# Performance work log

Hardware: AMD Instinct MI355X
Metric: run time of the kernel (lower is better)

The kernel has to match this reference:

```python
import jax, jax.numpy as jnp
import numpy as np

EMBED_DIM = 1024
NUM_HEADS = 16
HEAD_DIM = EMBED_DIM // NUM_HEADS


def setup_inputs() -> dict:
    key = jax.random.key(0)
    ks = jax.random.split(key, 9)
    s = 1.0 / np.sqrt(EMBED_DIM)
    X = jax.random.normal(ks[0], (4, 2048, EMBED_DIM), dtype=jnp.float32)
    # Linear weights stored as [in, out] for x @ W + b
    Wq = jax.random.uniform(ks[1], (EMBED_DIM, EMBED_DIM), jnp.float32, -s, s)
    bq = jax.random.uniform(ks[2], (EMBED_DIM,), jnp.float32, -s, s)
    Wk = jax.random.uniform(ks[3], (EMBED_DIM, EMBED_DIM), jnp.float32, -s, s)
    bk = jax.random.uniform(ks[4], (EMBED_DIM,), jnp.float32, -s, s)
    Wv = jax.random.uniform(ks[5], (EMBED_DIM, EMBED_DIM), jnp.float32, -s, s)
    bv = jax.random.uniform(ks[6], (EMBED_DIM,), jnp.float32, -s, s)
    Wo = jax.random.uniform(ks[7], (EMBED_DIM, EMBED_DIM), jnp.float32, -s, s)
    bo = jax.random.uniform(ks[8], (EMBED_DIM,), jnp.float32, -s, s)
    return {"X": X, "Wq": Wq, "bq": bq, "Wk": Wk, "bk": bk,
            "Wv": Wv, "bv": bv, "Wo": Wo, "bo": bo}


def reference(X, Wq, bq, Wk, bk, Wv, bv, Wo, bo):
    B, S, _ = X.shape
    def split_heads(t):  # [B,S,E] -> [B,H,S,D]
        return t.reshape(B, S, NUM_HEADS, HEAD_DIM).transpose(0, 2, 1, 3)
    Q = split_heads(X @ Wq + bq)
    K = split_heads(X @ Wk + bk)
    V = split_heads(X @ Wv + bv)
    scale = 1.0 / np.sqrt(HEAD_DIM).astype(np.float32)
    scores = jnp.einsum('bhqd,bhkd->bhqk', Q, K) * scale
    probs = jax.nn.softmax(scores, axis=-1)
    attn = jnp.einsum('bhqk,bhkd->bhqd', probs, V)  # [B,H,S,D]
    combined = attn.transpose(0, 2, 1, 3).reshape(B, S, EMBED_DIM)
    return combined @ Wo + bo
```

## Files before the change

kernel.cpp:

```cpp
#include <hip/hip_runtime.h>
#include <hip/hip_bf16.h>

#define EMBED 1024
#define NHEADS 16
#define HDIM 64
#define SEQ 2048
#define BATCH 4
#define ROWS (BATCH * SEQ)

typedef __attribute__((ext_vector_type(8))) short bf16x8;
typedef __attribute__((ext_vector_type(4))) float f32x4;
typedef __attribute__((ext_vector_type(2))) float f32x2;
typedef __attribute__((ext_vector_type(16))) float f32x16;
typedef __attribute__((ext_vector_type(4))) unsigned int u32x4;
typedef __attribute__((ext_vector_type(2))) unsigned int u32x2;
typedef __attribute__((ext_vector_type(2))) int i32x2;
typedef unsigned int u32;

#define SL2E 0.18033688011112042f

__device__ __forceinline__ short f2bf(float f) {
    u32 u = __builtin_bit_cast(u32, f) + 0x8000u;
    return (short)(u >> 16);
}

__device__ __forceinline__ u32 pkbf(float a, float b) {
    u32 ua = __builtin_bit_cast(u32, a) + 0x8000u;
    u32 ub = __builtin_bit_cast(u32, b) + 0x8000u;
    return __builtin_amdgcn_perm(ua, ub, 0x03020706u);
}

__device__ __forceinline__ float fexp2(float x) {
#if __has_builtin(__builtin_amdgcn_exp2f)
    return __builtin_amdgcn_exp2f(x);
#else
    return exp2f(x);
#endif
}

__device__ __forceinline__ void async16(const void* g, void* l) {
    __builtin_amdgcn_global_load_lds((const __attribute__((address_space(1))) u32*)g,
                                     (__attribute__((address_space(3))) u32*)l, 16, 0, 0);
}

__global__ __launch_bounds__(256) void convert_f32_bf16(const float* __restrict__ in,
                                                        short* __restrict__ out) {
    int i = (blockIdx.x * 256 + threadIdx.x) * 4;
    float4 v = *(const float4*)&in[i];
    u32x2 o = { pkbf(v.x, v.y), pkbf(v.z, v.w) };
    *(u32x2*)&out[i] = o;
}

__global__ __launch_bounds__(256) void transpose_w4(const float* __restrict__ W0,
                                                    const float* __restrict__ W1,
                                                    const float* __restrict__ W2,
                                                    const float* __restrict__ W3,
                                                    short* __restrict__ T0,
                                                    short* __restrict__ T1,
                                                    short* __restrict__ T2,
                                                    short* __restrict__ T3) {
    const int z = blockIdx.z;
    const float* W = (z == 0) ? W0 : (z == 1) ? W1 : (z == 2) ? W2 : W3;
    short* WT = (z == 0) ? T0 : (z == 1) ? T1 : (z == 2) ? T2 : T3;
    const float sc = (z == 0) ? SL2E : 1.0f;
    __shared__ float T[64][65];
    const int k0 = blockIdx.y * 64, n0 = blockIdx.x * 64;
    const int rr = threadIdx.x >> 4, cc = (threadIdx.x & 15) * 4;
    #pragma unroll
    for (int p = 0; p < 4; ++p) {
        int r = p * 16 + rr;
        float4 v = *(const float4*)&W[(size_t)(k0 + r) * EMBED + n0 + cc];
        T[r][cc] = v.x * sc; T[r][cc + 1] = v.y * sc; T[r][cc + 2] = v.z * sc; T[r][cc + 3] = v.w * sc;
    }
    __syncthreads();
    #pragma unroll
    for (int p = 0; p < 4; ++p) {
        int r = p * 16 + rr;
        u32x2 o = { pkbf(T[cc][r], T[cc + 1][r]), pkbf(T[cc + 2][r], T[cc + 3][r]) };
        *(u32x2*)&WT[(size_t)(n0 + r) * EMBED + k0 + cc] = o;
    }
}

__global__ __launch_bounds__(512, 2) void gemm256(const short* __restrict__ A,
                                                  const short* __restrict__ BT,
                                                  const float* __restrict__ b0,
                                                  const float* __restrict__ b1,
                                                  const float* __restrict__ b2,
                                                  void* __restrict__ C0,
                                                  void* __restrict__ C1,
                                                  void* __restrict__ C2,
                                                  int mode) {
    __shared__ short As[2][16384];
    __shared__ short Bs[2][16384];
    const int tid = threadIdx.x;
    const int wid = tid >> 6, lane = tid & 63;
    const int c16 = lane & 15, quad = lane >> 4, sw = c16 & 7;
    const int wm = wid >> 2, wn = wid & 3;
    const int rowblk = blockIdx.y * 256, colblk = blockIdx.x * 256;

    const int r0 = tid >> 3;
    const int g0 = (tid & 7) ^ (r0 & 7);
    const short* aS0 = A + (size_t)(rowblk + r0) * EMBED + g0 * 8;
    const short* bS0 = BT + (size_t)(colblk + r0) * EMBED + g0 * 8;

#define STAGE_A(SBUF, H, V) do { \
    const short* _s = aS0 + (size_t)(H) * 131072 + (V) * 64; \
    async16(_s,         &As[SBUF][(H) * 8192 + wid * 512]); \
    async16(_s + 65536, &As[SBUF][(H) * 8192 + wid * 512 + 4096]); \
} while (0)
#define STAGE_B(SBUF, H, V) do { \
    const short* _s = bS0 + (size_t)(H) * 131072 + (V) * 64; \
    async16(_s,         &Bs[SBUF][(H) * 8192 + wid * 512]); \
    async16(_s + 65536, &Bs[SBUF][(H) * 8192 + wid * 512 + 4096]); \
} while (0)

    f32x4 acc[8][4] = {};

#define PHASE(BUF, MH, NH, SAB, SBUF, SH, SV, VM) do { \
    bf16x8 af[4][2], bfv[2][2]; \
    _Pragma("unroll") \
    for (int fm = 0; fm < 4; ++fm) { \
        const int row = (MH) * 128 + wm * 64 + fm * 16 + c16; \
        _Pragma("unroll") \
        for (int ks = 0; ks < 2; ++ks) \
            af[fm][ks] = *(const bf16x8*)&As[BUF][row * 64 + ((ks * 4 + quad) ^ sw) * 8]; \
    } \
    _Pragma("unroll") \
    for (int fn = 0; fn < 2; ++fn) { \
        const int rowb = (NH) * 128 + wn * 32 + fn * 16 + c16; \
        _Pragma("unroll") \
        for (int ks = 0; ks < 2; ++ks) \
            bfv[fn][ks] = *(const bf16x8*)&Bs[BUF][rowb * 64 + ((ks * 4 + quad) ^ sw) * 8]; \
    } \
    if ((SAB) == 0) STAGE_A(SBUF, SH, SV); else STAGE_B(SBUF, SH, SV); \
    __builtin_amdgcn_s_barrier(); \
    asm volatile("s_waitcnt lgkmcnt(0)" ::: "memory"); \
    __builtin_amdgcn_s_setprio(1); \
    _Pragma("unroll") \
    for (int fm = 0; fm < 4; ++fm) \
        _Pragma("unroll") \
        for (int fn = 0; fn < 2; ++fn) \
            _Pragma("unroll") \
            for (int ks = 0; ks < 2; ++ks) \
                acc[(MH) * 4 + fm][(NH) * 2 + fn] = \
                    __builtin_amdgcn_mfma_f32_16x16x32_bf16(af[fm][ks], bfv[fn][ks], \
                        acc[(MH) * 4 + fm][(NH) * 2 + fn], 0, 0, 0); \
    __builtin_amdgcn_s_setprio(0); \
    if (VM) asm volatile("s_waitcnt vmcnt(4)" ::: "memory"); \
    __builtin_amdgcn_s_barrier(); \
} while (0)

    STAGE_A(0, 0, 0); STAGE_B(0, 0, 0);
    STAGE_A(0, 1, 0); STAGE_B(0, 1, 0);
    STAGE_A(1, 0, 1); STAGE_B(1, 0, 1);
    asm volatile("s_waitcnt vmcnt(4)" ::: "memory");
    __builtin_amdgcn_s_barrier();

    #pragma unroll 1
    for (int it = 0; it < 8; ++it) {
        const int u = 2 * it;
        const int v1 = u + 1, v2 = (u + 2) & 15, v3 = (u + 3) & 15;
        PHASE(0, 0, 0, 0, 1, 1, v1, 0);
        PHASE(0, 0, 1, 1, 1, 1, v1, 0);
        PHASE(0, 1, 0, 0, 0, 0, v2, 0);
        PHASE(0, 1, 1, 1, 0, 0, v2, 1);
        PHASE(1, 0, 0, 0, 0, 1, v2, 0);
        PHASE(1, 0, 1, 1, 0, 1, v2, 0);
        PHASE(1, 1, 0, 0, 1, 0, v3, 0);
        PHASE(1, 1, 1, 1, 1, 0, v3, 1);
    }

    asm volatile("s_waitcnt vmcnt(0)" ::: "memory");

    const int rb0 = rowblk + wm * 64 + quad * 4;
    const int cb0 = wn * 32 + c16;
    if (mode == 0) {
        const int z = colblk >> 10;
        const int cm = colblk & 1023;
        const float* bias = (z == 0) ? b0 : (z == 1) ? b1 : b2;
        if (z == 2) {
            short* Vt = (short*)C2;
            #pragma unroll
            for (int m = 0; m < 8; ++m) {
                const int row = rb0 + (m >> 2) * 128 + (m & 3) * 16;
                const int b = row >> 11, s = row & 2047;
                #pragma unroll
                for (int n = 0; n < 4; ++n) {
                    const int cv = cm + cb0 + (n >> 1) * 128 + (n & 1) * 16;
                    const int head = cv >> 6, d = cv & 63;
                    const float bv = bias[cv];
                    u32x2 o = { pkbf(acc[m][n][0] + bv, acc[m][n][1] + bv),
                                pkbf(acc[m][n][2] + bv, acc[m][n][3] + bv) };
                    *(u32x2*)&Vt[((size_t)(b * NHEADS + head) * HDIM + d) * SEQ + s] = o;
                }
            }
        } else {
            short* Cq = (short*)((z == 0) ? C0 : C1);
            const float bsc = (z == 0) ? SL2E : 1.0f;
            #pragma unroll
            for (int m = 0; m < 8; ++m) {
                const int row = rb0 + (m >> 2) * 128 + (m & 3) * 16;
                #pragma unroll
                for (int n = 0; n < 4; ++n) {
                    const int col = cm + cb0 + (n >> 1) * 128 + (n & 1) * 16;
                    const float bv = bias[col] * bsc;
                    #pragma unroll
                    for (int r = 0; r < 4; ++r)
                        Cq[(size_t)(row + r) * EMBED + col] = f2bf(acc[m][n][r] + bv);
                }
            }
        }
    } else {
        float* Co = (float*)C0;
        #pragma unroll
        for (int m = 0; m < 8; ++m) {
            const int row = rb0 + (m >> 2) * 128 + (m & 3) * 16;
            #pragma unroll
            for (int n = 0; n < 4; ++n) {
                const int col = colblk + cb0 + (n >> 1) * 128 + (n & 1) * 16;
                const float bv = b0[col];
                #pragma unroll
                for (int r = 0; r < 4; ++r)
                    Co[(size_t)(row + r) * EMBED + col] = acc[m][n][r] + bv;
            }
        }
    }
#undef PHASE
#undef STAGE_A
#undef STAGE_B
}

__global__ __launch_bounds__(256, 3) void attn_mfma(const short* __restrict__ Qb,
                                                    const short* __restrict__ Kb,
                                                    const short* __restrict__ Vt,
                                                    short* __restrict__ Ob) {
    __shared__ short SH[8192];
    short* Ks = SH;
    short* Vs = SH + 4096;
    const int tid = threadIdx.x;
    const int wave = tid >> 6, lane = tid & 63;
    const int l31 = lane & 31, h = lane >> 5;
    const int swz = l31 & 7;
    const int bh = blockIdx.y;
    const int b = bh >> 4, hd = bh & 15;
    const size_t base = (size_t)b * SEQ * EMBED + (size_t)hd * HDIM;
    const size_t vbase = (size_t)bh * HDIM * SEQ;
    const int q0 = blockIdx.x * 128;

    bf16x8 qf[4];
    #pragma unroll
    for (int ks = 0; ks < 4; ++ks)
        qf[ks] = *(const bf16x8*)&Qb[base + (size_t)(q0 + wave * 32 + l31) * EMBED + ks * 16 + h * 8];

    const short* kp[2];
    const short* vp[2];
    int ldofs[2];
    #pragma unroll
    for (int it = 0; it < 2; ++it) {
        int ci = (it * 4 + wave) * 64 + lane;
        int row = ci >> 3, g = (ci & 7) ^ (row & 7);
        kp[it] = Kb + base + (size_t)row * EMBED + g * 8;
        vp[it] = Vt + vbase + (size_t)row * SEQ + g * 8;
        ldofs[it] = (it * 4 + wave) * 512;
    }

    f32x16 O[2] = {};
    f32x2 ls = {0.0f, 0.0f};

    for (int kt = 0; kt < SEQ / 64; ++kt) {
        #pragma unroll
        for (int it = 0; it < 2; ++it) {
            async16(kp[it], &Ks[ldofs[it]]);
            async16(vp[it], &Vs[ldofs[it]]);
            kp[it] += 64 * EMBED;
            vp[it] += 64;
        }
        __syncthreads();

        f32x16 st[2] = {};
        #pragma unroll
        for (int nt = 0; nt < 2; ++nt)
            #pragma unroll
            for (int ks = 0; ks < 4; ++ks) {
                bf16x8 ak = *(const bf16x8*)&Ks[(nt * 32 + l31) * 64 + ((ks * 2 + h) ^ swz) * 8];
                st[nt] = __builtin_amdgcn_mfma_f32_32x32x16_bf16(ak, qf[ks], st[nt], 0, 0, 0);
            }

        u32 pk[2][8];
        #pragma unroll
        for (int nt = 0; nt < 2; ++nt)
            #pragma unroll
            for (int i = 0; i < 8; ++i) {
                float e0 = fexp2(st[nt][2 * i]), e1 = fexp2(st[nt][2 * i + 1]);
                f32x2 e = { e0, e1 };
                ls += e;
                pk[nt][i] = pkbf(e0, e1);
            }

        #pragma unroll
        for (int ks = 0; ks < 4; ++ks) {
            const int nt = ks >> 1, bs = (ks & 1) * 4;
            u32x4 fr;
#if __has_builtin(__builtin_amdgcn_permlane32_swap)
            i32x2 sA = __builtin_amdgcn_permlane32_swap((int)pk[nt][bs + 0], (int)pk[nt][bs + 2], false, false);
            i32x2 sB = __builtin_amdgcn_permlane32_swap((int)pk[nt][bs + 1], (int)pk[nt][bs + 3], false, false);
            fr.x = (u32)sA.x; fr.y = (u32)sB.x; fr.z = (u32)sA.y; fr.w = (u32)sB.y;
#else
            u32 s0 = h ? pk[nt][bs + 0] : pk[nt][bs + 2];
            u32 s1 = h ? pk[nt][bs + 1] : pk[nt][bs + 3];
            u32 r0 = (u32)__shfl_xor((int)s0, 32);
            u32 r1 = (u32)__shfl_xor((int)s1, 32);
            fr.x = h ? r0 : pk[nt][bs + 0];
            fr.y = h ? r1 : pk[nt][bs + 1];
            fr.z = h ? pk[nt][bs + 2] : r0;
            fr.w = h ? pk[nt][bs + 3] : r1;
#endif
            bf16x8 pf = __builtin_bit_cast(bf16x8, fr);
            #pragma unroll
            for (int mt = 0; mt < 2; ++mt) {
                bf16x8 vf = *(const bf16x8*)&Vs[(mt * 32 + l31) * 64 + ((ks * 2 + h) ^ swz) * 8];
                O[mt] = __builtin_amdgcn_mfma_f32_32x32x16_bf16(vf, pf, O[mt], 0, 0, 0);
            }
        }
        __syncthreads();
    }

    float lsum = ls.x + ls.y;
    lsum += __shfl_xor(lsum, 32);
    float inv = 1.0f / lsum;

    const int wbase = wave * 2048;
    #pragma unroll
    for (int mt = 0; mt < 2; ++mt)
        #pragma unroll
        for (int m = 0; m < 4; ++m) {
            u32x2 wv;
            wv.x = pkbf(O[mt][4 * m + 0] * inv, O[mt][4 * m + 1] * inv);
            wv.y = pkbf(O[mt][4 * m + 2] * inv, O[mt][4 * m + 3] * inv);
            int u = mt * 8 + 2 * m + h;
            int su = u ^ ((l31 & 7) << 1);
            *(u32x2*)&SH[wbase + l31 * 64 + su * 4] = wv;
        }
    __syncthreads();
    #pragma unroll
    for (int p = 0; p < 4; ++p) {
        int ci = p * 256 + tid;
        int wq = ci >> 8, rem = ci & 255;
        int r = rem >> 3, cch = rem & 7;
        int su = (2 * cch) ^ ((r & 7) << 1);
        bf16x8 val = *(const bf16x8*)&SH[wq * 2048 + r * 64 + su * 4];
        *(bf16x8*)&Ob[base + (size_t)(q0 + wq * 32 + r) * EMBED + cch * 8] = val;
    }
}

extern "C" void kernel_launch(void* const* d_in, const int* in_sizes, int n_in,
                              void* d_out, int out_size, void* d_ws, size_t ws_size,
                              hipStream_t stream)
{
    const float* X  = (const float*)d_in[0];
    const float* Wq = (const float*)d_in[1];
    const float* bq = (const float*)d_in[2];
    const float* Wk = (const float*)d_in[3];
    const float* bk = (const float*)d_in[4];
    const float* Wv = (const float*)d_in[5];
    const float* bv = (const float*)d_in[6];
    const float* Wo = (const float*)d_in[7];
    const float* bo = (const float*)d_in[8];
    float* out = (float*)d_out;

    const size_t NE = (size_t)ROWS * EMBED;
    short* Xbf = (short*)d_ws;
    short* Qb  = Xbf + NE;
    short* Kb  = Qb + NE;
    short* Vtb = Kb + NE;
    short* WqT = Vtb + NE;
    short* WkT = WqT + (size_t)EMBED * EMBED;
    short* WvT = WkT + (size_t)EMBED * EMBED;
    short* WoT = WvT + (size_t)EMBED * EMBED;

    convert_f32_bf16<<<(ROWS * EMBED) / 1024, 256, 0, stream>>>(X, Xbf);
    dim3 gw(16, 16, 4);
    transpose_w4<<<gw, 256, 0, stream>>>(Wq, Wk, Wv, Wo, WqT, WkT, WvT, WoT);

    dim3 gq(12, 32, 1);
    gemm256<<<gq, 512, 0, stream>>>(Xbf, WqT, bq, bk, bv, Qb, Kb, Vtb, 0);

    dim3 gt(SEQ / 128, BATCH * NHEADS);
    attn_mfma<<<gt, 256, 0, stream>>>(Qb, Kb, Vtb, Qb);

    dim3 gg(4, 32, 1);
    gemm256<<<gg, 512, 0, stream>>>(Qb, WoT, bo, bo, bo, out, out, out, 1);
}
```

Before: 311.3 us.

## Reorder GEMM phases to reuse A/B fragments and use 128x64 kernel for output projection

Restructures the 256x256 GEMM main loop so that A and B register fragments are loaded once and reused across consecutive MFMA phases (even/odd B buffers, snake order), with adjusted staging order and vmcnt depth. This cuts LDS reads per phase. The output projection now uses a new simpler 128x64-tile kernel with more blocks (16x64 grid) instead of the 4x32 grid of 256-tiles, to improve CU occupancy for the smaller GEMM. The new kernel has no software pipelining and may be less efficient per tile.

```diff
diff --git a/kernel.cpp b/kernel.cpp
--- a/kernel.cpp
+++ b/kernel.cpp
@@ -115,59 +115,65 @@
 } while (0)
 
     f32x4 acc[8][4] = {};
-
-#define PHASE(BUF, MH, NH, SAB, SBUF, SH, SV, VM) do { \
-    bf16x8 af[4][2], bfv[2][2]; \
+    bf16x8 aU[4][2], bE[2][2], bO[2][2];
+
+#define LDA(BUF, MH) do { \
     _Pragma("unroll") \
     for (int fm = 0; fm < 4; ++fm) { \
         const int row = (MH) * 128 + wm * 64 + fm * 16 + c16; \
         _Pragma("unroll") \
         for (int ks = 0; ks < 2; ++ks) \
-            af[fm][ks] = *(const bf16x8*)&As[BUF][row * 64 + ((ks * 4 + quad) ^ sw) * 8]; \
+            aU[fm][ks] = *(const bf16x8*)&As[BUF][row * 64 + ((ks * 4 + quad) ^ sw) * 8]; \
     } \
+} while (0)
+#define LDB(BUF, NH, DST) do { \
     _Pragma("unroll") \
     for (int fn = 0; fn < 2; ++fn) { \
         const int rowb = (NH) * 128 + wn * 32 + fn * 16 + c16; \
         _Pragma("unroll") \
         for (int ks = 0; ks < 2; ++ks) \
-            bfv[fn][ks] = *(const bf16x8*)&Bs[BUF][rowb * 64 + ((ks * 4 + quad) ^ sw) * 8]; \
+            DST[fn][ks] = *(const bf16x8*)&Bs[BUF][rowb * 64 + ((ks * 4 + quad) ^ sw) * 8]; \
     } \
-    if ((SAB) == 0) STAGE_A(SBUF, SH, SV); else STAGE_B(SBUF, SH, SV); \
-    __builtin_amdgcn_s_barrier(); \
-    asm volatile("s_waitcnt lgkmcnt(0)" ::: "memory"); \
-    __builtin_amdgcn_s_setprio(1); \
+} while (0)
+#define MM(MB, NB, BM_) do { \
     _Pragma("unroll") \
     for (int fm = 0; fm < 4; ++fm) \
         _Pragma("unroll") \
         for (int fn = 0; fn < 2; ++fn) \
             _Pragma("unroll") \
             for (int ks = 0; ks < 2; ++ks) \
-                acc[(MH) * 4 + fm][(NH) * 2 + fn] = \
-                    __builtin_amdgcn_mfma_f32_16x16x32_bf16(af[fm][ks], bfv[fn][ks], \
-                        acc[(MH) * 4 + fm][(NH) * 2 + fn], 0, 0, 0); \
+                acc[(MB) + fm][(NB) + fn] = \
+                    __builtin_amdgcn_mfma_f32_16x16x32_bf16(aU[fm][ks], BM_[fn][ks], \
+                        acc[(MB) + fm][(NB) + fn], 0, 0, 0); \
+} while (0)
+#define PH_MID() do { \
+    __builtin_amdgcn_s_barrier(); \
+    asm volatile("s_waitcnt lgkmcnt(0)" ::: "memory"); \
+    __builtin_amdgcn_s_setprio(1); \
+} while (0)
+#define PH_END(VM) do { \
     __builtin_amdgcn_s_setprio(0); \
-    if (VM) asm volatile("s_waitcnt vmcnt(4)" ::: "memory"); \
+    if (VM) asm volatile("s_waitcnt vmcnt(6)" ::: "memory"); \
     __builtin_amdgcn_s_barrier(); \
 } while (0)
 
-    STAGE_A(0, 0, 0); STAGE_B(0, 0, 0);
-    STAGE_A(0, 1, 0); STAGE_B(0, 1, 0);
-    STAGE_A(1, 0, 1); STAGE_B(1, 0, 1);
-    asm volatile("s_waitcnt vmcnt(4)" ::: "memory");
+    STAGE_B(0, 0, 0); STAGE_A(0, 0, 0); STAGE_A(0, 1, 0); STAGE_B(0, 1, 0);
+    STAGE_B(1, 0, 1); STAGE_A(1, 0, 1); STAGE_A(1, 1, 1);
+    asm volatile("s_waitcnt vmcnt(6)" ::: "memory");
     __builtin_amdgcn_s_barrier();
 
     #pragma unroll 1
     for (int it = 0; it < 8; ++it) {
         const int u = 2 * it;
         const int v1 = u + 1, v2 = (u + 2) & 15, v3 = (u + 3) & 15;
-        PHASE(0, 0, 0, 0, 1, 1, v1, 0);
-        PHASE(0, 0, 1, 1, 1, 1, v1, 0);
-        PHASE(0, 1, 0, 0, 0, 0, v2, 0);
-        PHASE(0, 1, 1, 1, 0, 0, v2, 1);
-        PHASE(1, 0, 0, 0, 0, 1, v2, 0);
-        PHASE(1, 0, 1, 1, 0, 1, v2, 0);
-        PHASE(1, 1, 0, 0, 1, 0, v3, 0);
-        PHASE(1, 1, 1, 1, 1, 0, v3, 1);
+        LDA(0, 0); LDB(0, 0, bE); STAGE_B(1, 1, v1); PH_MID(); MM(0, 0, bE); PH_END(0);
+        LDB(0, 1, bO);            STAGE_B(0, 0, v2); PH_MID(); MM(0, 2, bO); PH_END(0);
+        LDA(0, 1);                STAGE_A(0, 0, v2); PH_MID(); MM(4, 2, bO); PH_END(0);
+                 STAGE_A(0, 1, v2); PH_MID(); MM(4, 0, bE); PH_END(1);
+        LDA(1, 0); LDB(1, 0, bE); STAGE_B(0, 1, v2); PH_MID(); MM(0, 0, bE); PH_END(0);
+        LDB(1, 1, bO);            STAGE_B(1, 0, v3); PH_MID(); MM(0, 2, bO); PH_END(0);
+        LDA(1, 1);                STAGE_A(1, 0, v3); PH_MID(); MM(4, 2, bO); PH_END(0);
+                 STAGE_A(1, 1, v3); PH_MID(); MM(4, 0, bE); PH_END(1);
     }
 
     asm volatile("s_waitcnt vmcnt(0)" ::: "memory");
@@ -225,9 +231,101 @@
             }
         }
     }
-#undef PHASE
+#undef PH_END
+#undef PH_MID
+#undef MM
+#undef LDB
+#undef LDA
 #undef STAGE_A
 #undef STAGE_B
+}
+
+__global__ __launch_bounds__(256, 5) void gemm_bf16_128(const short* __restrict__ A,
+                                                        const short* __restrict__ BT0,
+                                                        const short* __restrict__ BT1,
+                                                        const short* __restrict__ BT2,
+                                                        const float* __restrict__ b0,
+                                                        const float* __restrict__ b1,
+                                                        const float* __restrict__ b2,
+                                                        void* __restrict__ C0,
+                                                        void* __restrict__ C1,
+                                                        void* __restrict__ C2,
+                                                        int mode) {
+    const int z = blockIdx.z;
+    const short* BT = (z == 0) ? BT0 : (z == 1) ? BT1 : BT2;
+    const float* bias = (z == 0) ? b0 : (z == 1) ? b1 : b2;
+    const float bsc = (mode == 0 && z == 0) ? SL2E : 1.0f;
+    __shared__ short As[128 * 64];
+    __shared__ short Bs[64 * 64];
+    const int tid = threadIdx.x;
+    const int wave = tid >> 6, lane = tid & 63;
+    const int c = lane & 15, quad = lane >> 4;
+    const int sw = c & 7;
+    const int row0 = blockIdx.y * 128, col0 = blockIdx.x * 64;
+    f32x4 acc[2][4] = {};
+    for (int k0 = 0; k0 < EMBED; k0 += 64) {
+        #pragma unroll
+        for (int it = 0; it < 4; ++it) {
+            int ci = (it * 4 + wave) * 64 + lane;
+            int row = ci >> 3, g = (ci & 7) ^ (row & 7);
+            async16(&A[(size_t)(row0 + row) * EMBED + k0 + g * 8], &As[(it * 4 + wave) * 512]);
+        }
+        #pragma unroll
+        for (int it = 0; it < 2; ++it) {
+            int ci = (it * 4 + wave) * 64 + lane;
+            int row = ci >> 3, g = (ci & 7) ^ (row & 7);
+            async16(&BT[(size_t)(col0 + row) * EMBED + k0 + g * 8], &Bs[(it * 4 + wave) * 512]);
+        }
+        __syncthreads();
+        #pragma unroll
+        for (int ks = 0; ks < 2; ++ks) {
+            bf16x8 af[2], bfr[4];
+            #pragma unroll
+            for (int i = 0; i < 2; ++i)
+                af[i] = *(const bf16x8*)&As[(wave * 32 + i * 16 + c) * 64 + ((ks * 4 + quad) ^ sw) * 8];
+            #pragma unroll
+            for (int j = 0; j < 4; ++j)
+                bfr[j] = *(const bf16x8*)&Bs[(j * 16 + c) * 64 + ((ks * 4 + quad) ^ sw) * 8];
+            #pragma unroll
+            for (int i = 0; i < 2; ++i)
+                #pragma unroll
+                for (int j = 0; j < 4; ++j)
+                    acc[i][j] = __builtin_amdgcn_mfma_f32_16x16x32_bf16(af[i], bfr[j], acc[i][j], 0, 0, 0);
+        }
+        __syncthreads();
+    }
+    if (mode == 0 && z == 2) {
+        short* Vt = (short*)C2;
+        const int b = row0 >> 11, s0 = (row0 & 2047) + wave * 32;
+        const int bh = b * NHEADS + blockIdx.x;
+        #pragma unroll
+        for (int i = 0; i < 2; ++i)
+            #pragma unroll
+            for (int j = 0; j < 4; ++j) {
+                int d = j * 16 + c;
+                float bv = bias[col0 + d];
+                int s = s0 + i * 16 + quad * 4;
+                u32x2 o = { pkbf(acc[i][j][0] + bv, acc[i][j][1] + bv),
+                            pkbf(acc[i][j][2] + bv, acc[i][j][3] + bv) };
+                *(u32x2*)&Vt[((size_t)bh * HDIM + d) * SEQ + s] = o;
+            }
+    } else {
+        void* Cout = (z == 0) ? C0 : (z == 1) ? C1 : C2;
+        #pragma unroll
+        for (int i = 0; i < 2; ++i)
+            #pragma unroll
+            for (int j = 0; j < 4; ++j) {
+                int colb = col0 + j * 16 + c;
+                float bv = bias[colb] * bsc;
+                #pragma unroll
+                for (int r = 0; r < 4; ++r) {
+                    int row = row0 + wave * 32 + i * 16 + quad * 4 + r;
+                    float v = acc[i][j][r] + bv;
+                    if (mode == 0) ((short*)Cout)[(size_t)row * EMBED + colb] = f2bf(v);
+                    else           ((float*)Cout)[(size_t)row * EMBED + colb] = v;
+                }
+            }
+    }
 }
 
 __global__ __launch_bounds__(256, 3) void attn_mfma(const short* __restrict__ Qb,
@@ -388,6 +486,7 @@
     dim3 gt(SEQ / 128, BATCH * NHEADS);
     attn_mfma<<<gt, 256, 0, stream>>>(Qb, Kb, Vtb, Qb);
 
-    dim3 gg(4, 32, 1);
-    gemm256<<<gg, 512, 0, stream>>>(Qb, WoT, bo, bo, bo, out, out, out, 1);
-}
+    dim3 gg(EMBED / 64, ROWS / 128, 1);
+    gemm_bf16_128<<<gg, 256, 0, stream>>>(Qb, WoT, WoT, WoT, bo, bo, bo,
+                                          out, out, out, 1);
+}
```

Result: faster. 276.8 us (-11.1%).

## Shrink GEMM tile to 128x256 with swizzled block order; double-buffer attention K/V

Applied to the files above, without the earlier changes.

The projection GEMMs move from 256x256 to 128x256 tiles with a new phase schedule that reuses A/B fragments across MFMA groups. Block indices are remapped in groups of 8 so neighbouring blocks share operands in cache. The grids double to fill more CUs. The attention kernel now double-buffers K/V tiles in LDS so the next tile loads while the current one computes, and it raises wave priority around the MFMA sections. The costs are more blocks with lower per-block reuse in the GEMM and twice the LDS use in attention, which may lower occupancy.

```diff
diff --git a/kernel.cpp b/kernel.cpp
--- a/kernel.cpp
+++ b/kernel.cpp
@@ -81,99 +81,116 @@
     }
 }
 
-__global__ __launch_bounds__(512, 2) void gemm256(const short* __restrict__ A,
-                                                  const short* __restrict__ BT,
-                                                  const float* __restrict__ b0,
-                                                  const float* __restrict__ b1,
-                                                  const float* __restrict__ b2,
-                                                  void* __restrict__ C0,
-                                                  void* __restrict__ C1,
-                                                  void* __restrict__ C2,
-                                                  int mode) {
-    __shared__ short As[2][16384];
+__global__ __launch_bounds__(512, 2) void gemm_p128(const short* __restrict__ A,
+                                                    const short* __restrict__ BT,
+                                                    const float* __restrict__ b0,
+                                                    const float* __restrict__ b1,
+                                                    const float* __restrict__ b2,
+                                                    void* __restrict__ C0,
+                                                    void* __restrict__ C1,
+                                                    void* __restrict__ C2,
+                                                    int mode) {
+    __shared__ short As[2][8192];
     __shared__ short Bs[2][16384];
     const int tid = threadIdx.x;
-    const int wid = tid >> 6, lane = tid & 63;
+    const int lane = tid & 63;
+    const int wid = tid >> 6;
     const int c16 = lane & 15, quad = lane >> 4, sw = c16 & 7;
     const int wm = wid >> 2, wn = wid & 3;
-    const int rowblk = blockIdx.y * 256, colblk = blockIdx.x * 256;
+    const int gx = gridDim.x;
+    const int hid = blockIdx.y * gx + blockIdx.x;
+    const int cpx = (gx * gridDim.y) >> 3;
+    const int tle = (hid & 7) * cpx + (hid >> 3);
+    const int bx = tle % gx, by = tle / gx;
+    const int rowblk = by * 128, colblk = bx * 256;
 
     const int r0 = tid >> 3;
     const int g0 = (tid & 7) ^ (r0 & 7);
     const short* aS0 = A + (size_t)(rowblk + r0) * EMBED + g0 * 8;
     const short* bS0 = BT + (size_t)(colblk + r0) * EMBED + g0 * 8;
 
-#define STAGE_A(SBUF, H, V) do { \
-    const short* _s = aS0 + (size_t)(H) * 131072 + (V) * 64; \
-    async16(_s,         &As[SBUF][(H) * 8192 + wid * 512]); \
-    async16(_s + 65536, &As[SBUF][(H) * 8192 + wid * 512 + 4096]); \
-} while (0)
-#define STAGE_B(SBUF, H, V) do { \
-    const short* _s = bS0 + (size_t)(H) * 131072 + (V) * 64; \
-    async16(_s,         &Bs[SBUF][(H) * 8192 + wid * 512]); \
-    async16(_s + 65536, &Bs[SBUF][(H) * 8192 + wid * 512 + 4096]); \
-} while (0)
-
-    f32x4 acc[8][4] = {};
-
-#define PHASE(BUF, MH, NH, SAB, SBUF, SH, SV, VM) do { \
-    bf16x8 af[4][2], bfv[2][2]; \
+#define STAGE_A(SBUF, V) do { \
+    const short* _s = aS0 + (V) * 64; \
+    async16(_s,         &As[SBUF][tid * 8]); \
+    async16(_s + 65536, &As[SBUF][tid * 8 + 4096]); \
+} while (0)
+#define STAGE_B0(SBUF, V) do { \
+    const short* _s = bS0 + (V) * 64; \
+    async16(_s,         &Bs[SBUF][tid * 8]); \
+    async16(_s + 65536, &Bs[SBUF][tid * 8 + 4096]); \
+} while (0)
+#define STAGE_B1(SBUF, V) do { \
+    const short* _s = bS0 + 131072 + (V) * 64; \
+    async16(_s,         &Bs[SBUF][tid * 8 + 8192]); \
+    async16(_s + 65536, &Bs[SBUF][tid * 8 + 12288]); \
+} while (0)
+
+    f32x4 acc[4][4] = {};
+    bf16x8 aU[2][2], bE[2][2], bO[2][2];
+
+#define LDA(BUF, MH) do { \
     _Pragma("unroll") \
-    for (int fm = 0; fm < 4; ++fm) { \
-        const int row = (MH) * 128 + wm * 64 + fm * 16 + c16; \
+    for (int fm = 0; fm < 2; ++fm) { \
+        const int row = wm * 64 + (MH) * 32 + fm * 16 + c16; \
         _Pragma("unroll") \
         for (int ks = 0; ks < 2; ++ks) \
-            af[fm][ks] = *(const bf16x8*)&As[BUF][row * 64 + ((ks * 4 + quad) ^ sw) * 8]; \
+            aU[fm][ks] = *(const bf16x8*)&As[BUF][row * 64 + ((ks * 4 + quad) ^ sw) * 8]; \
     } \
+} while (0)
+#define LDB(BUF, NH, DST) do { \
     _Pragma("unroll") \
     for (int fn = 0; fn < 2; ++fn) { \
-        const int rowb = (NH) * 128 + wn * 32 + fn * 16 + c16; \
+        const int col = wn * 64 + (NH) * 32 + fn * 16 + c16; \
         _Pragma("unroll") \
         for (int ks = 0; ks < 2; ++ks) \
-            bfv[fn][ks] = *(const bf16x8*)&Bs[BUF][rowb * 64 + ((ks * 4 + quad) ^ sw) * 8]; \
+            DST[fn][ks] = *(const bf16x8*)&Bs[BUF][col * 64 + ((ks * 4 + quad) ^ sw) * 8]; \
     } \
-    if ((SAB) == 0) STAGE_A(SBUF, SH, SV); else STAGE_B(SBUF, SH, SV); \
-    __builtin_amdgcn_s_barrier(); \
-    asm volatile("s_waitcnt lgkmcnt(0)" ::: "memory"); \
-    __builtin_amdgcn_s_setprio(1); \
+} while (0)
+#define MM(MB, NB, BM_) do { \
     _Pragma("unroll") \
-    for (int fm = 0; fm < 4; ++fm) \
+    for (int fm = 0; fm < 2; ++fm) \
         _Pragma("unroll") \
         for (int fn = 0; fn < 2; ++fn) \
             _Pragma("unroll") \
             for (int ks = 0; ks < 2; ++ks) \
-                acc[(MH) * 4 + fm][(NH) * 2 + fn] = \
-                    __builtin_amdgcn_mfma_f32_16x16x32_bf16(af[fm][ks], bfv[fn][ks], \
-                        acc[(MH) * 4 + fm][(NH) * 2 + fn], 0, 0, 0); \
+                acc[(MB) + fm][(NB) + fn] = \
+                    __builtin_amdgcn_mfma_f32_16x16x32_bf16(aU[fm][ks], BM_[fn][ks], \
+                        acc[(MB) + fm][(NB) + fn], 0, 0, 0); \
+} while (0)
+#define PH_MID() do { \
+    __builtin_amdgcn_s_barrier(); \
+    asm volatile("s_waitcnt lgkmcnt(0)" ::: "memory"); \
+    __builtin_amdgcn_s_setprio(1); \
+} while (0)
+#define PH_END(VM) do { \
     __builtin_amdgcn_s_setprio(0); \
-    if (VM) asm volatile("s_waitcnt vmcnt(4)" ::: "memory"); \
+    if (VM) asm volatile("s_waitcnt vmcnt(6)" ::: "memory"); \
     __builtin_amdgcn_s_barrier(); \
 } while (0)
 
-    STAGE_A(0, 0, 0); STAGE_B(0, 0, 0);
-    STAGE_A(0, 1, 0); STAGE_B(0, 1, 0);
-    STAGE_A(1, 0, 1); STAGE_B(1, 0, 1);
-    asm volatile("s_waitcnt vmcnt(4)" ::: "memory");
+    STAGE_B0(0, 0); STAGE_A(0, 0); STAGE_B1(0, 0);
+    STAGE_B0(1, 1); STAGE_A(1, 1); STAGE_B1(1, 1);
+    asm volatile("s_waitcnt vmcnt(6)" ::: "memory");
     __builtin_amdgcn_s_barrier();
 
     #pragma unroll 1
     for (int it = 0; it < 8; ++it) {
         const int u = 2 * it;
-        const int v1 = u + 1, v2 = (u + 2) & 15, v3 = (u + 3) & 15;
-        PHASE(0, 0, 0, 0, 1, 1, v1, 0);
-        PHASE(0, 0, 1, 1, 1, 1, v1, 0);
-        PHASE(0, 1, 0, 0, 0, 0, v2, 0);
-        PHASE(0, 1, 1, 1, 0, 0, v2, 1);
-        PHASE(1, 0, 0, 0, 0, 1, v2, 0);
-        PHASE(1, 0, 1, 1, 0, 1, v2, 0);
-        PHASE(1, 1, 0, 0, 1, 0, v3, 0);
-        PHASE(1, 1, 1, 1, 1, 0, v3, 1);
+        const int v2 = (u + 2) & 15, v3 = (u + 3) & 15;
+        LDA(0, 0); LDB(0, 0, bE);                     PH_MID(); MM(0, 0, bE); PH_END(0);
+        LDB(0, 1, bO);            STAGE_B0(0, v2);    PH_MID(); MM(0, 2, bO); PH_END(0);
+        LDA(0, 1);                STAGE_B1(0, v2);    PH_MID(); MM(2, 2, bO); PH_END(0);
+                 STAGE_A(0, v2);     PH_MID(); MM(2, 0, bE); PH_END(1);
+        LDA(1, 0); LDB(1, 0, bE);                     PH_MID(); MM(0, 0, bE); PH_END(0);
+        LDB(1, 1, bO);            STAGE_B0(1, v3);    PH_MID(); MM(0, 2, bO); PH_END(0);
+        LDA(1, 1);                STAGE_B1(1, v3);    PH_MID(); MM(2, 2, bO); PH_END(0);
+                 STAGE_A(1, v3);     PH_MID(); MM(2, 0, bE); PH_END(1);
     }
 
     asm volatile("s_waitcnt vmcnt(0)" ::: "memory");
 
     const int rb0 = rowblk + wm * 64 + quad * 4;
-    const int cb0 = wn * 32 + c16;
+    const int cb0 = wn * 64 + c16;
     if (mode == 0) {
         const int z = colblk >> 10;
         const int cm = colblk & 1023;
@@ -181,12 +198,12 @@
         if (z == 2) {
             short* Vt = (short*)C2;
             #pragma unroll
-            for (int m = 0; m < 8; ++m) {
-                const int row = rb0 + (m >> 2) * 128 + (m & 3) * 16;
+            for (int m = 0; m < 4; ++m) {
+                const int row = rb0 + (m >> 1) * 32 + (m & 1) * 16;
                 const int b = row >> 11, s = row & 2047;
                 #pragma unroll
                 for (int n = 0; n < 4; ++n) {
-                    const int cv = cm + cb0 + (n >> 1) * 128 + (n & 1) * 16;
+                    const int cv = cm + cb0 + (n >> 1) * 32 + (n & 1) * 16;
                     const int head = cv >> 6, d = cv & 63;
                     const float bv = bias[cv];
                     u32x2 o = { pkbf(acc[m][n][0] + bv, acc[m][n][1] + bv),
@@ -198,11 +215,11 @@
             short* Cq = (short*)((z == 0) ? C0 : C1);
             const float bsc = (z == 0) ? SL2E : 1.0f;
             #pragma unroll
-            for (int m = 0; m < 8; ++m) {
-                const int row = rb0 + (m >> 2) * 128 + (m & 3) * 16;
+            for (int m = 0; m < 4; ++m) {
+                const int row = rb0 + (m >> 1) * 32 + (m & 1) * 16;
                 #pragma unroll
                 for (int n = 0; n < 4; ++n) {
-                    const int col = cm + cb0 + (n >> 1) * 128 + (n & 1) * 16;
+                    const int col = cm + cb0 + (n >> 1) * 32 + (n & 1) * 16;
                     const float bv = bias[col] * bsc;
                     #pragma unroll
                     for (int r = 0; r < 4; ++r)
@@ -213,11 +230,11 @@
     } else {
         float* Co = (float*)C0;
         #pragma unroll
-        for (int m = 0; m < 8; ++m) {
-            const int row = rb0 + (m >> 2) * 128 + (m & 3) * 16;
+        for (int m = 0; m < 4; ++m) {
+            const int row = rb0 + (m >> 1) * 32 + (m & 1) * 16;
             #pragma unroll
             for (int n = 0; n < 4; ++n) {
-                const int col = colblk + cb0 + (n >> 1) * 128 + (n & 1) * 16;
+                const int col = colblk + cb0 + (n >> 1) * 32 + (n & 1) * 16;
                 const float bv = b0[col];
                 #pragma unroll
                 for (int r = 0; r < 4; ++r)
@@ -225,27 +242,32 @@
             }
         }
     }
-#undef PHASE
+#undef PH_END
+#undef PH_MID
+#undef MM
+#undef LDB
+#undef LDA
+#undef STAGE_B1
+#undef STAGE_B0
 #undef STAGE_A
-#undef STAGE_B
 }
 
 __global__ __launch_bounds__(256, 3) void attn_mfma(const short* __restrict__ Qb,
                                                     const short* __restrict__ Kb,
                                                     const short* __restrict__ Vt,
                                                     short* __restrict__ Ob) {
-    __shared__ short SH[8192];
-    short* Ks = SH;
-    short* Vs = SH + 4096;
+    __shared__ short SH[16384];
     const int tid = threadIdx.x;
     const int wave = tid >> 6, lane = tid & 63;
     const int l31 = lane & 31, h = lane >> 5;
     const int swz = l31 & 7;
-    const int bh = blockIdx.y;
+    const int hid = blockIdx.y * 16 + blockIdx.x;
+    const int tle = (hid & 7) * 128 + (hid >> 3);
+    const int qb = tle & 15, bh = tle >> 4;
     const int b = bh >> 4, hd = bh & 15;
     const size_t base = (size_t)b * SEQ * EMBED + (size_t)hd * HDIM;
     const size_t vbase = (size_t)bh * HDIM * SEQ;
-    const int q0 = blockIdx.x * 128;
+    const int q0 = qb * 128;
 
     bf16x8 qf[4];
     #pragma unroll
@@ -267,17 +289,34 @@
     f32x16 O[2] = {};
     f32x2 ls = {0.0f, 0.0f};
 
+    #pragma unroll
+    for (int it = 0; it < 2; ++it) {
+        async16(kp[it], &SH[ldofs[it]]);
+        async16(vp[it], &SH[8192 + ldofs[it]]);
+        kp[it] += 64 * EMBED;
+        vp[it] += 64;
+    }
+    asm volatile("s_waitcnt vmcnt(0)" ::: "memory");
+    __builtin_amdgcn_s_barrier();
+
+    #pragma unroll 2
     for (int kt = 0; kt < SEQ / 64; ++kt) {
-        #pragma unroll
-        for (int it = 0; it < 2; ++it) {
-            async16(kp[it], &Ks[ldofs[it]]);
-            async16(vp[it], &Vs[ldofs[it]]);
-            kp[it] += 64 * EMBED;
-            vp[it] += 64;
+        const int bo = (kt & 1) * 4096;
+        const short* Ks = SH + bo;
+        const short* Vs = SH + 8192 + bo;
+        if (kt < SEQ / 64 - 1) {
+            const int nbo = 4096 - bo;
+            #pragma unroll
+            for (int it = 0; it < 2; ++it) {
+                async16(kp[it], &SH[nbo + ldofs[it]]);
+                async16(vp[it], &SH[8192 + nbo + ldofs[it]]);
+                kp[it] += 64 * EMBED;
+                vp[it] += 64;
+            }
         }
-        __syncthreads();
 
         f32x16 st[2] = {};
+        __builtin_amdgcn_s_setprio(1);
         #pragma unroll
         for (int nt = 0; nt < 2; ++nt)
             #pragma unroll
@@ -285,6 +324,7 @@
                 bf16x8 ak = *(const bf16x8*)&Ks[(nt * 32 + l31) * 64 + ((ks * 2 + h) ^ swz) * 8];
                 st[nt] = __builtin_amdgcn_mfma_f32_32x32x16_bf16(ak, qf[ks], st[nt], 0, 0, 0);
             }
+        __builtin_amdgcn_s_setprio(0);
 
         u32 pk[2][8];
         #pragma unroll
@@ -297,6 +337,7 @@
                 pk[nt][i] = pkbf(e0, e1);
             }
 
+        __builtin_amdgcn_s_setprio(1);
         #pragma unroll
         for (int ks = 0; ks < 4; ++ks) {
             const int nt = ks >> 1, bs = (ks & 1) * 4;
@@ -322,7 +363,10 @@
                 O[mt] = __builtin_amdgcn_mfma_f32_32x32x16_bf16(vf, pf, O[mt], 0, 0, 0);
             }
         }
-        __syncthreads();
+        __builtin_amdgcn_s_setprio(0);
+
+        asm volatile("s_waitcnt vmcnt(0)" ::: "memory");
+        __builtin_amdgcn_s_barrier();
     }
 
     float lsum = ls.x + ls.y;
@@ -382,12 +426,12 @@
     dim3 gw(16, 16, 4);
     transpose_w4<<<gw, 256, 0, stream>>>(Wq, Wk, Wv, Wo, WqT, WkT, WvT, WoT);
 
-    dim3 gq(12, 32, 1);
-    gemm256<<<gq, 512, 0, stream>>>(Xbf, WqT, bq, bk, bv, Qb, Kb, Vtb, 0);
+    dim3 gq(12, 64, 1);
+    gemm_p128<<<gq, 512, 0, stream>>>(Xbf, WqT, bq, bk, bv, Qb, Kb, Vtb, 0);
 
     dim3 gt(SEQ / 128, BATCH * NHEADS);
     attn_mfma<<<gt, 256, 0, stream>>>(Qb, Kb, Vtb, Qb);
 
-    dim3 gg(4, 32, 1);
-    gemm256<<<gg, 512, 0, stream>>>(Qb, WoT, bo, bo, bo, out, out, out, 1);
-}
+    dim3 gg(4, 64, 1);
+    gemm_p128<<<gg, 512, 0, stream>>>(Qb, WoT, bo, bo, bo, out, out, out, 1);
+}
```

After: 277.1 us. 11.0% less time.
